# Kernel optimization log

Measured on AMD Instinct MI355X. Metric: run time of the kernel, lower is better.

## Reference

```python
import jax, jax.numpy as jnp
import numpy as np

QMAX = 127.0  # 8-bit symmetric: levels in [-128, 127]


def _ste_round(v):
    # round with straight-through estimator (matches torch fake-quant training)
    return v + jax.lax.stop_gradient(jnp.round(v) - v)


def _act_fake_quant(x, clip_factor):
    # per-tensor symmetric fake quant with learnable clip (lac):
    # clip range = sigmoid(clip_factor) * max|x|
    scale = jax.nn.sigmoid(clip_factor) * jnp.max(jnp.abs(x)) / QMAX
    return jnp.clip(_ste_round(x / scale), -QMAX - 1.0, QMAX) * scale


def _weight_fake_quant(w):
    # per-output-channel symmetric fake quant; w: [out, in]
    scale = jnp.max(jnp.abs(w), axis=1, keepdims=True) / QMAX
    return jnp.clip(_ste_round(w / scale), -QMAX - 1.0, QMAX) * scale


def setup_inputs() -> dict:
    key = jax.random.key(0)
    k1, k2, k3, k4 = jax.random.split(key, 4)
    B, S, H, I = 8, 8192, 1024, 2816
    return {
        "x": jax.random.normal(k1, (B, S, H), dtype=jnp.float32),
        "clip_x": jnp.full((1,), 4.0, dtype=jnp.float32),     # sigmoid(4) ~ 0.982
        "clip_down": jnp.full((1,), 4.0, dtype=jnp.float32),
        "w_gate": jax.random.normal(k2, (I, H), dtype=jnp.float32) * 0.02,
        "w_up": jax.random.normal(k3, (I, H), dtype=jnp.float32) * 0.02,
        "w_down": jax.random.normal(k4, (H, I), dtype=jnp.float32) * 0.02,
    }


def reference(x, clip_x, clip_down, w_gate, w_up, w_down):
    # _trans_forward: quantize act -> gate/up quant-matmul -> SwiGLU -> quantize -> down quant-matmul
    xq = _act_fake_quant(x, clip_x[0])                       # [B,S,H]
    gate = jnp.einsum("bsh,ih->bsi", xq, _weight_fake_quant(w_gate))
    up = jnp.einsum("bsh,ih->bsi", xq, _weight_fake_quant(w_up))
    h = _act_fake_quant(jax.nn.silu(gate) * up, clip_down[0])  # [B,S,I]
    return jnp.einsum("bsi,hi->bsh", h, _weight_fake_quant(w_down))
```

## Files before the change

kernel.cpp:

```cpp
#include <hip/hip_runtime.h>
#include <stdint.h>

typedef __attribute__((ext_vector_type(4))) int i32x4;

typedef const __attribute__((address_space(1))) void gvoid_t;
typedef __attribute__((address_space(3))) void lvoid_t;

#define GLD16(g, l) __builtin_amdgcn_global_load_lds((gvoid_t*)(g), (lvoid_t*)(l), 16, 0, 0)
#define FENCE() asm volatile("" ::: "memory")
#define BARRIER() do { FENCE(); __builtin_amdgcn_s_barrier(); FENCE(); } while (0)
#define SCHEDB() __builtin_amdgcn_sched_barrier(0)
#define GATE(n) asm volatile("s_waitcnt vmcnt(" #n ")\n\ts_barrier" ::: "memory")

__device__ inline int q1mul(float x, float r) {
    return (int)fminf(fmaxf(rintf(x * r), -128.f), 127.f);
}
__device__ inline int q1div(float x, float s) {
    return (int)fminf(fmaxf(rintf(x / s), -128.f), 127.f);
}
__device__ inline int pack4(float4 v, float r) {
    return (q1mul(v.x, r) & 255) | ((q1mul(v.y, r) & 255) << 8) |
           ((q1mul(v.z, r) & 255) << 16) | ((q1mul(v.w, r) & 255) << 24);
}

__global__ void k_absmax(const float* __restrict__ x, size_t n4, unsigned int* __restrict__ out) {
    size_t S = (size_t)gridDim.x * blockDim.x;
    size_t i = (size_t)blockIdx.x * blockDim.x + threadIdx.x;
    const float4* x4 = (const float4*)x;
    float m0 = 0.f, m1 = 0.f, m2 = 0.f, m3 = 0.f;
    for (; i + 3 * S < n4; i += 4 * S) {
        float4 v0 = x4[i], v1 = x4[i + S], v2 = x4[i + 2 * S], v3 = x4[i + 3 * S];
        m0 = fmaxf(m0, fmaxf(fmaxf(fabsf(v0.x), fabsf(v0.y)), fmaxf(fabsf(v0.z), fabsf(v0.w))));
        m1 = fmaxf(m1, fmaxf(fmaxf(fabsf(v1.x), fabsf(v1.y)), fmaxf(fabsf(v1.z), fabsf(v1.w))));
        m2 = fmaxf(m2, fmaxf(fmaxf(fabsf(v2.x), fabsf(v2.y)), fmaxf(fabsf(v2.z), fabsf(v2.w))));
        m3 = fmaxf(m3, fmaxf(fmaxf(fabsf(v3.x), fabsf(v3.y)), fmaxf(fabsf(v3.z), fabsf(v3.w))));
    }
    for (; i < n4; i += S) {
        float4 v = x4[i];
        m0 = fmaxf(m0, fmaxf(fmaxf(fabsf(v.x), fabsf(v.y)), fmaxf(fabsf(v.z), fabsf(v.w))));
    }
    float m = fmaxf(fmaxf(m0, m1), fmaxf(m2, m3));
    #pragma unroll
    for (int off = 32; off > 0; off >>= 1) m = fmaxf(m, __shfl_xor(m, off, 64));
    if ((threadIdx.x & 63) == 0) atomicMax(out, __float_as_uint(m));
}

__global__ void k_scale(const float* __restrict__ clip, const unsigned int* __restrict__ maxbits,
                        float* __restrict__ s_out) {
    float m = __uint_as_float(*maxbits);
    float sig = 1.f / (1.f + expf(-clip[0]));
    float s = sig * m / 127.f;
    s_out[0] = s;
    s_out[1] = 1.f / s;
}

__global__ void k_quant_f32_i8(const float* __restrict__ in, int4* __restrict__ out,
                               const float* __restrict__ sptr, size_t n16) {
    float r = sptr[1];
    size_t S = (size_t)gridDim.x * blockDim.x;
    size_t i = (size_t)blockIdx.x * blockDim.x + threadIdx.x;
    const float4* in4 = (const float4*)in;
    for (; i < n16; i += S) {
        float4 v0 = in4[4 * i], v1 = in4[4 * i + 1], v2 = in4[4 * i + 2], v3 = in4[4 * i + 3];
        int4 o;
        o.x = pack4(v0, r); o.y = pack4(v1, r); o.z = pack4(v2, r); o.w = pack4(v3, r);
        out[i] = o;
    }
}

__global__ void k_quant_h16_i8(const short* __restrict__ h16, const float* __restrict__ sblk,
                               const float* __restrict__ sh, int4* __restrict__ qh, size_t nchunks) {
    const float rh = sh[1] * (1.f / 32766.f);
    size_t S = (size_t)gridDim.x * blockDim.x;
    size_t i = (size_t)blockIdx.x * blockDim.x + threadIdx.x;
    for (; i < nchunks; i += S) {
        int row = (int)(i / 176);
        int col = (int)(i - (size_t)row * 176) * 16;
        float f = sblk[(row >> 8) * 22 + (col >> 7)] * rh;
        const int4* p = (const int4*)(h16 + (size_t)row * 2816 + col);
        int4 lo = p[0], hi = p[1];
        int w[8] = {lo.x, lo.y, lo.z, lo.w, hi.x, hi.y, hi.z, hi.w};
        int ob[4];
        #pragma unroll
        for (int j = 0; j < 4; ++j) {
            int q0 = q1mul((float)(short)(w[2 * j] & 0xFFFF), f);
            int q1 = q1mul((float)(short)(w[2 * j] >> 16), f);
            int q2 = q1mul((float)(short)(w[2 * j + 1] & 0xFFFF), f);
            int q3 = q1mul((float)(short)(w[2 * j + 1] >> 16), f);
            ob[j] = (q0 & 255) | ((q1 & 255) << 8) | ((q2 & 255) << 16) | ((q3 & 255) << 24);
        }
        int4 o; o.x = ob[0]; o.y = ob[1]; o.z = ob[2]; o.w = ob[3];
        qh[i] = o;
    }
}

__global__ void k_quant_w_i8(const float* __restrict__ W, int8_t* __restrict__ Q,
                             float* __restrict__ srow, int cols) {
    int row = blockIdx.x;
    const float* w = W + (size_t)row * cols;
    float m = 0.f;
    for (int c = threadIdx.x; c < cols; c += 256) m = fmaxf(m, fabsf(w[c]));
    #pragma unroll
    for (int off = 32; off > 0; off >>= 1) m = fmaxf(m, __shfl_xor(m, off, 64));
    __shared__ float red[4];
    if ((threadIdx.x & 63) == 0) red[threadIdx.x >> 6] = m;
    __syncthreads();
    if (threadIdx.x == 0) {
        float mm = fmaxf(fmaxf(red[0], red[1]), fmaxf(red[2], red[3]));
        red[0] = mm / 127.f;
        srow[row] = mm / 127.f;
    }
    __syncthreads();
    float s = red[0];
    for (int c = threadIdx.x; c < cols; c += 256)
        Q[(size_t)row * cols + c] = (int8_t)q1div(w[c], s);
}

#define MFMA_G1(AF, BG, BU, OFF)                                                              \
    _Pragma("unroll")                                                                         \
    for (int mi = 0; mi < 4; ++mi) {                                                          \
        _Pragma("unroll")                                                                     \
        for (int ni = 0; ni < 2; ++ni) {                                                      \
            accg[(OFF) + mi][ni] = __builtin_amdgcn_mfma_i32_16x16x64_i8(AF[mi], BG[ni], accg[(OFF) + mi][ni], 0, 0, 0); \
            accu[(OFF) + mi][ni] = __builtin_amdgcn_mfma_i32_16x16x64_i8(AF[mi], BU[ni], accu[(OFF) + mi][ni], 0, 0, 0); \
        }                                                                                     \
    }

__global__ __launch_bounds__(512, 2) void k_gemm1_i8(
    const int8_t* __restrict__ Aq, const int8_t* __restrict__ Bg, const int8_t* __restrict__ Bu,
    const float* __restrict__ sg, const float* __restrict__ su, const float* __restrict__ sx,
    short* __restrict__ H16, float* __restrict__ sblk, unsigned int* __restrict__ maxh,
    int nt_base)
{
    constexpr int K = 1024, N = 2816, NT = K / 128, BUF = 65536;
    __shared__ int8_t lds[2 * BUF];

    const int wgl = (int)blockIdx.x >> 3;
    const int xcd = (int)blockIdx.x & 7;
    const int mtspan = (int)(gridDim.x >> 3) / 11;
    const int mt = xcd * mtspan + wgl / 11;
    const int nt = nt_base + wgl % 11;
    const int m0 = mt * 256, n0 = nt * 128;
    const int tid = threadIdx.x;
    const int wid = tid >> 6, lane = tid & 63;
    const int wm = wid >> 2, wn = wid & 3;
    const int lr = lane & 15, lk = lane >> 4;

    const int srow = tid >> 2;
    const int scol = ((tid & 3) ^ ((srow >> 1) & 3)) << 4;
    const int8_t* gA0 = Aq + (size_t)(m0 + srow) * K + scol;
    const int8_t* gA1 = gA0 + (size_t)128 * K;
    const int8_t* gG  = Bg + (size_t)(n0 + srow) * K + scol;
    const int8_t* gU  = Bu + (size_t)(n0 + srow) * K + scol;
    const int ldst = wid << 10;

    const int swz = (lk ^ ((lr >> 1) & 3)) << 4;
    const int aoff = (wm * 128 + lr) * 64 + swz;
    const int boffG = 32768 + (wn * 32 + lr) * 64 + swz;
    const int boffU = 40960 + (wn * 32 + lr) * 64 + swz;

    i32x4 accg[8][2] = {};
    i32x4 accu[8][2] = {};
    i32x4 aA[4], aB[4], bgA[2], buA[2], bgB[2], buB[2];

    {
        int8_t* Lw = &lds[0];
        GLD16(gA0,      Lw + ldst);         GLD16(gA1,      Lw + 8192  + ldst);
        GLD16(gG,       Lw + 32768 + ldst); GLD16(gU,       Lw + 40960 + ldst);
        GLD16(gA0 + 64, Lw + 16384 + ldst); GLD16(gA1 + 64, Lw + 24576 + ldst);
        GLD16(gG  + 64, Lw + 49152 + ldst); GLD16(gU  + 64, Lw + 57344 + ldst);
    }
    GATE(4);
    {
        const int8_t* Lr = &lds[0];
        #pragma unroll
        for (int mi = 0; mi < 4; ++mi) aA[mi] = *(const i32x4*)(Lr + aoff + mi * 1024);
        #pragma unroll
        for (int ni = 0; ni < 2; ++ni) {
            bgA[ni] = *(const i32x4*)(Lr + boffG + ni * 1024);
            buA[ni] = *(const i32x4*)(Lr + boffU + ni * 1024);
        }
    }

    for (int t = 0; t < NT; ++t) {
        const bool st = (t + 1 < NT);
        const int8_t* Lr = &lds[(t & 1) * BUF];
        int8_t* Lw = &lds[((t + 1) & 1) * BUF];
        const size_t kk = (size_t)(t + 1) * 128;

        #pragma unroll
        for (int mi = 0; mi < 4; ++mi) aB[mi] = *(const i32x4*)(Lr + aoff + 4096 + mi * 1024);
        if (st) { GLD16(gA0 + kk, Lw + ldst); GLD16(gA1 + kk, Lw + 8192 + ldst); }
        SCHEDB();
        __builtin_amdgcn_s_setprio(1);
        MFMA_G1(aA, bgA, buA, 0);
        __builtin_amdgcn_s_setprio(0);
        if (st) { GATE(2); } else { GATE(0); }

        #pragma unroll
        for (int mi = 0; mi < 4; ++mi) aA[mi] = *(const i32x4*)(Lr + 16384 + aoff + mi * 1024);
        #pragma unroll
        for (int ni = 0; ni < 2; ++ni) {
            bgB[ni] = *(const i32x4*)(Lr + 16384 + boffG + ni * 1024);
            buB[ni] = *(const i32x4*)(Lr + 16384 + boffU + ni * 1024);
        }
        if (st) { GLD16(gG + kk, Lw + 32768 + ldst); GLD16(gU + kk, Lw + 40960 + ldst); }
        SCHEDB();
        __builtin_amdgcn_s_setprio(1);
        MFMA_G1(aB, bgA, buA, 4);
        __builtin_amdgcn_s_setprio(0);

        #pragma unroll
        for (int mi = 0; mi < 4; ++mi) aB[mi] = *(const i32x4*)(Lr + 16384 + aoff + 4096 + mi * 1024);
        if (st) { GLD16(gA0 + kk + 64, Lw + 16384 + ldst); GLD16(gA1 + kk + 64, Lw + 24576 + ldst);
                  GLD16(gG + kk + 64, Lw + 49152 + ldst);  GLD16(gU + kk + 64, Lw + 57344 + ldst); }
        SCHEDB();
        __builtin_amdgcn_s_setprio(1);
        MFMA_G1(aA, bgB, buB, 0);
        __builtin_amdgcn_s_setprio(0);
        if (st) { GATE(4); } else { GATE(0); }

        if (st) {
            #pragma unroll
            for (int mi = 0; mi < 4; ++mi) aA[mi] = *(const i32x4*)(Lw + aoff + mi * 1024);
            #pragma unroll
            for (int ni = 0; ni < 2; ++ni) {
                bgA[ni] = *(const i32x4*)(Lw + boffG + ni * 1024);
                buA[ni] = *(const i32x4*)(Lw + boffU + ni * 1024);
            }
        }
        SCHEDB();
        __builtin_amdgcn_s_setprio(1);
        MFMA_G1(aB, bgB, buB, 4);
        __builtin_amdgcn_s_setprio(0);
    }
    BARRIER();

    const float s_x = sx[0];
    float lmax = 0.f;
    #pragma unroll
    for (int ni = 0; ni < 2; ++ni) {
        const int nl = wn * 32 + ni * 16 + lr;
        const float fg = s_x * sg[n0 + nl];
        const float fu = s_x * su[n0 + nl];
        #pragma unroll
        for (int mi = 0; mi < 8; ++mi) {
            const int rowb = wm * 128 + mi * 16 + lk * 4;
            #pragma unroll
            for (int r = 0; r < 4; ++r) {
                float g = (float)accg[mi][ni][r] * fg;
                float u = (float)accu[mi][ni][r] * fu;
                float h = g * u / (1.f + expf(-g));
                *(float*)(lds + ((rowb + r) << 9) + (nl << 2)) = h;
                lmax = fmaxf(lmax, fabsf(h));
            }
        }
    }
    #pragma unroll
    for (int off = 32; off > 0; off >>= 1) lmax = fmaxf(lmax, __shfl_xor(lmax, off, 64));
    unsigned int* slot = (unsigned int*)&sblk[mt * 22 + nt];
    if (lane == 0) atomicMax(slot, __float_as_uint(lmax));
    BARRIER();
    const float bmax = __uint_as_float(*slot);
    if (tid == 0) atomicMax(maxh, __float_as_uint(bmax));
    const float qs = 32766.f / fmaxf(bmax, 1e-20f);
    uint* H16u = (uint*)H16;
    #pragma unroll
    for (int k = 0; k < 32; ++k) {
        const int fidx = 2 * (tid + k * 512);
        const int row = fidx >> 7, col = fidx & 127;
        const float2 hv = *(const float2*)(lds + (fidx << 2));
        const int s0 = (int)rintf(hv.x * qs), s1 = (int)rintf(hv.y * qs);
        H16u[((size_t)(m0 + row) * N + n0 + col) >> 1] = (s0 & 0xFFFF) | (s1 << 16);
    }
}

#define MFMA_G2(AF, BF, OFF)                                                                  \
    _Pragma("unroll")                                                                         \
    for (int mi = 0; mi < 4; ++mi) {                                                          \
        _Pragma("unroll")                                                                     \
        for (int ni = 0; ni < 4; ++ni)                                                        \
            acc[(OFF) + mi][ni] = __builtin_amdgcn_mfma_i32_16x16x64_i8(AF[mi], BF[ni], acc[(OFF) + mi][ni], 0, 0, 0); \
    }

__global__ __launch_bounds__(512, 2) void k_gemm2_i8(
    const int8_t* __restrict__ Aq, const int8_t* __restrict__ Bw,
    const float* __restrict__ sw, const float* __restrict__ sh,
    float* __restrict__ Out)
{
    constexpr int K = 2816, N = 1024, NT = K / 128, BUF = 65536;
    __shared__ int8_t lds[2 * BUF];

    const int chunk = gridDim.x >> 3;
    const int wg = ((int)blockIdx.x & 7) * chunk + ((int)blockIdx.x >> 3);
    const int mt = wg >> 2, nt = wg & 3;
    const int m0 = mt * 256, n0 = nt * 256;
    const int tid = threadIdx.x;
    const int wid = tid >> 6, lane = tid & 63;
    const int wm = wid >> 2, wn = wid & 3;
    const int lr = lane & 15, lk = lane >> 4;

    const int srow = tid >> 2;
    const int scol = ((tid & 3) ^ ((srow >> 1) & 3)) << 4;
    const int8_t* gA0 = Aq + (size_t)(m0 + srow) * K + scol;
    const int8_t* gA1 = gA0 + (size_t)128 * K;
    const int8_t* gB0 = Bw + (size_t)(n0 + srow) * K + scol;
    const int8_t* gB1 = gB0 + (size_t)128 * K;
    const int ldst = wid << 10;

    const int swz = (lk ^ ((lr >> 1) & 3)) << 4;
    const int aoff = (wm * 128 + lr) * 64 + swz;
    const int boff = 32768 + (wn * 64 + lr) * 64 + swz;

    i32x4 acc[8][4] = {};
    i32x4 aA[4], aB[4], bA[4], bB[4];

    {
        int8_t* Lw = &lds[0];
        GLD16(gA0,      Lw + ldst);         GLD16(gA1,      Lw + 8192  + ldst);
        GLD16(gB0,      Lw + 32768 + ldst); GLD16(gB1,      Lw + 40960 + ldst);
        GLD16(gA0 + 64, Lw + 16384 + ldst); GLD16(gA1 + 64, Lw + 24576 + ldst);
        GLD16(gB0 + 64, Lw + 49152 + ldst); GLD16(gB1 + 64, Lw + 57344 + ldst);
    }
    GATE(4);
    {
        const int8_t* Lr = &lds[0];
        #pragma unroll
        for (int mi = 0; mi < 4; ++mi) aA[mi] = *(const i32x4*)(Lr + aoff + mi * 1024);
        #pragma unroll
        for (int ni = 0; ni < 4; ++ni) bA[ni] = *(const i32x4*)(Lr + boff + ni * 1024);
    }

    for (int t = 0; t < NT; ++t) {
        const bool st = (t + 1 < NT);
        const int8_t* Lr = &lds[(t & 1) * BUF];
        int8_t* Lw = &lds[((t + 1) & 1) * BUF];
        const size_t kk = (size_t)(t + 1) * 128;

        #pragma unroll
        for (int mi = 0; mi < 4; ++mi) aB[mi] = *(const i32x4*)(Lr + aoff + 4096 + mi * 1024);
        if (st) { GLD16(gA0 + kk, Lw + ldst); GLD16(gA1 + kk, Lw + 8192 + ldst); }
        SCHEDB();
        __builtin_amdgcn_s_setprio(1);
        MFMA_G2(aA, bA, 0);
        __builtin_amdgcn_s_setprio(0);
        if (st) { GATE(2); } else { GATE(0); }

        #pragma unroll
        for (int mi = 0; mi < 4; ++mi) aA[mi] = *(const i32x4*)(Lr + 16384 + aoff + mi * 1024);
        #pragma unroll
        for (int ni = 0; ni < 4; ++ni) bB[ni] = *(const i32x4*)(Lr + 16384 + boff + ni * 1024);
        if (st) { GLD16(gB0 + kk, Lw + 32768 + ldst); GLD16(gB1 + kk, Lw + 40960 + ldst); }
        SCHEDB();
        __builtin_amdgcn_s_setprio(1);
        MFMA_G2(aB, bA, 4);
        __builtin_amdgcn_s_setprio(0);

        #pragma unroll
        for (int mi = 0; mi < 4; ++mi) aB[mi] = *(const i32x4*)(Lr + 16384 + aoff + 4096 + mi * 1024);
        if (st) { GLD16(gA0 + kk + 64, Lw + 16384 + ldst); GLD16(gA1 + kk + 64, Lw + 24576 + ldst);
                  GLD16(gB0 + kk + 64, Lw + 49152 + ldst); GLD16(gB1 + kk + 64, Lw + 57344 + ldst); }
        SCHEDB();
        __builtin_amdgcn_s_setprio(1);
        MFMA_G2(aA, bB, 0);
        __builtin_amdgcn_s_setprio(0);
        if (st) { GATE(4); } else { GATE(0); }

        if (st) {
            #pragma unroll
            for (int mi = 0; mi < 4; ++mi) aA[mi] = *(const i32x4*)(Lw + aoff + mi * 1024);
            #pragma unroll
            for (int ni = 0; ni < 4; ++ni) bA[ni] = *(const i32x4*)(Lw + boff + ni * 1024);
        }
        SCHEDB();
        __builtin_amdgcn_s_setprio(1);
        MFMA_G2(aB, bB, 4);
        __builtin_amdgcn_s_setprio(0);
    }

    const float s_h = sh[0];
    #pragma unroll
    for (int ni = 0; ni < 4; ++ni) {
        const int n = n0 + wn * 64 + ni * 16 + lr;
        const float f = s_h * sw[n];
        #pragma unroll
        for (int mi = 0; mi < 8; ++mi) {
            const int mb = m0 + wm * 128 + mi * 16 + lk * 4;
            #pragma unroll
            for (int r = 0; r < 4; ++r)
                Out[(size_t)(mb + r) * N + n] = (float)acc[mi][ni][r] * f;
        }
    }
}

extern "C" void kernel_launch(void* const* d_in, const int* in_sizes, int n_in,
                              void* d_out, int out_size, void* d_ws, size_t ws_size,
                              hipStream_t stream) {
    const float* x       = (const float*)d_in[0];
    const float* clip_x  = (const float*)d_in[1];
    const float* clip_dn = (const float*)d_in[2];
    const float* w_gate  = (const float*)d_in[3];
    const float* w_up    = (const float*)d_in[4];
    const float* w_down  = (const float*)d_in[5];
    float* out = (float*)d_out;

    const int Hd = 1024, Id = 2816;
    const int M = in_sizes[0] / Hd;
    const size_t nx = (size_t)M * Hd;
    const size_t nh = (size_t)M * Id;

    char* ws = (char*)d_ws;
    size_t off = 0;
    auto alloc = [&](size_t bytes) -> char* {
        char* p = ws + off;
        off = (off + bytes + 255) & ~(size_t)255;
        return p;
    };
    unsigned int* max_slots = (unsigned int*)alloc(8);
    float* sxp = (float*)alloc(8);
    float* shp = (float*)alloc(8);
    int8_t* qx  = (int8_t*)alloc(nx);
    int8_t* qwg = (int8_t*)alloc((size_t)Id * Hd);
    int8_t* qwu = (int8_t*)alloc((size_t)Id * Hd);
    int8_t* qwd = (int8_t*)alloc((size_t)Hd * Id);
    float* swg = (float*)alloc((size_t)Id * 4);
    float* swu = (float*)alloc((size_t)Id * 4);
    float* swd = (float*)alloc((size_t)Hd * 4);
    int8_t* qh = (int8_t*)alloc(nh);
    short* h16 = (short*)alloc(nh * 2);
    const size_t sblk_bytes = (size_t)(M / 256) * 22 * 4;
    float* sblk = (float*)alloc(sblk_bytes);

    hipMemsetAsync(max_slots, 0, 8, stream);
    hipMemsetAsync(sblk, 0, sblk_bytes, stream);

    k_absmax<<<4096, 256, 0, stream>>>(x, nx / 4, &max_slots[0]);
    k_scale<<<1, 1, 0, stream>>>(clip_x, &max_slots[0], sxp);
    k_quant_f32_i8<<<2048, 256, 0, stream>>>(x, (int4*)qx, sxp, nx / 16);
    k_quant_w_i8<<<Id, 256, 0, stream>>>(w_gate, qwg, swg, Hd);
    k_quant_w_i8<<<Id, 256, 0, stream>>>(w_up, qwu, swu, Hd);
    k_quant_w_i8<<<Hd, 256, 0, stream>>>(w_down, qwd, swd, Id);

    const int g1grid = (M / 256) * 11;
    k_gemm1_i8<<<g1grid, 512, 0, stream>>>(qx, qwg, qwu, swg, swu, sxp, h16, sblk, &max_slots[1], 0);
    k_gemm1_i8<<<g1grid, 512, 0, stream>>>(qx, qwg, qwu, swg, swu, sxp, h16, sblk, &max_slots[1], 11);
    k_scale<<<1, 1, 0, stream>>>(clip_dn, &max_slots[1], shp);
    k_quant_h16_i8<<<4096, 256, 0, stream>>>(h16, sblk, shp, (int4*)qh, nh / 16);

    k_gemm2_i8<<<(M / 256) * (Hd / 256), 512, 0, stream>>>(qh, qwd, swd, shp, out);
}
```

Before: 1.137 ms.

## Switch int8 GEMMs from 16x16x64 to 32x32x32 MFMA tiles

Both int8 GEMM kernels now use the 32x32x32 i8 MFMA instruction instead of 16x16x64. The LDS fragment addressing, the per-wave register tiling and the epilogue row/column mapping are rewritten to match the 32x32 output layout. Each operand fragment feeds more output per instruction, which is meant to cut the LDS reads and instruction count per FLOP. In exchange the epilogue store pattern changes and the new LDS read swizzle may bring bank conflicts.

```diff
diff --git a/kernel.cpp b/kernel.cpp
--- a/kernel.cpp
+++ b/kernel.cpp
@@ -2,6 +2,7 @@
 #include <stdint.h>
 
 typedef __attribute__((ext_vector_type(4))) int i32x4;
+typedef __attribute__((ext_vector_type(16))) int i32x16;
 
 typedef const __attribute__((address_space(1))) void gvoid_t;
 typedef __attribute__((address_space(3))) void lvoid_t;
@@ -116,14 +117,11 @@
         Q[(size_t)row * cols + c] = (int8_t)q1div(w[c], s);
 }
 
-#define MFMA_G1(AF, BG, BU, OFF)                                                              \
+#define MFMA8_G1(AF, BG, BU)                                                                  \
     _Pragma("unroll")                                                                         \
-    for (int mi = 0; mi < 4; ++mi) {                                                          \
-        _Pragma("unroll")                                                                     \
-        for (int ni = 0; ni < 2; ++ni) {                                                      \
-            accg[(OFF) + mi][ni] = __builtin_amdgcn_mfma_i32_16x16x64_i8(AF[mi], BG[ni], accg[(OFF) + mi][ni], 0, 0, 0); \
-            accu[(OFF) + mi][ni] = __builtin_amdgcn_mfma_i32_16x16x64_i8(AF[mi], BU[ni], accu[(OFF) + mi][ni], 0, 0, 0); \
-        }                                                                                     \
+    for (int m = 0; m < 4; ++m) {                                                             \
+        accg[m] = __builtin_amdgcn_mfma_i32_32x32x32_i8(AF[m], BG, accg[m], 0, 0, 0);         \
+        accu[m] = __builtin_amdgcn_mfma_i32_32x32x32_i8(AF[m], BU, accu[m], 0, 0, 0);         \
     }
 
 __global__ __launch_bounds__(512, 2) void k_gemm1_i8(
@@ -144,7 +142,8 @@
     const int tid = threadIdx.x;
     const int wid = tid >> 6, lane = tid & 63;
     const int wm = wid >> 2, wn = wid & 3;
-    const int lr = lane & 15, lk = lane >> 4;
+    const int l31 = lane & 31, l5 = lane >> 5;
+    const int lp = (l31 >> 1) & 3;
 
     const int srow = tid >> 2;
     const int scol = ((tid & 3) ^ ((srow >> 1) & 3)) << 4;
@@ -154,14 +153,18 @@
     const int8_t* gU  = Bu + (size_t)(n0 + srow) * K + scol;
     const int ldst = wid << 10;
 
-    const int swz = (lk ^ ((lr >> 1) & 3)) << 4;
-    const int aoff = (wm * 128 + lr) * 64 + swz;
-    const int boffG = 32768 + (wn * 32 + lr) * 64 + swz;
-    const int boffU = 40960 + (wn * 32 + lr) * 64 + swz;
-
-    i32x4 accg[8][2] = {};
-    i32x4 accu[8][2] = {};
-    i32x4 aA[4], aB[4], bgA[2], buA[2], bgB[2], buB[2];
+    const int F0 = ((l5 ^ lp) << 4);
+    const int F1 = (((2 + l5) ^ lp) << 4);
+    const int F2 = 16384 + F0, F3 = 16384 + F1;
+    int aR[4];
+    #pragma unroll
+    for (int m = 0; m < 4; ++m) aR[m] = (wm * 128 + m * 32 + l31) * 64;
+    const int bRg = 32768 + (wn * 32 + l31) * 64;
+    const int bRu = bRg + 8192;
+
+    i32x16 accg[4] = {};
+    i32x16 accu[4] = {};
+    i32x4 aA[4], aB[4], bgA, buA, bgB, buB;
 
     {
         int8_t* Lw = &lds[0];
@@ -174,12 +177,9 @@
     {
         const int8_t* Lr = &lds[0];
         #pragma unroll
-        for (int mi = 0; mi < 4; ++mi) aA[mi] = *(const i32x4*)(Lr + aoff + mi * 1024);
-        #pragma unroll
-        for (int ni = 0; ni < 2; ++ni) {
-            bgA[ni] = *(const i32x4*)(Lr + boffG + ni * 1024);
-            buA[ni] = *(const i32x4*)(Lr + boffU + ni * 1024);
-        }
+        for (int m = 0; m < 4; ++m) aA[m] = *(const i32x4*)(Lr + aR[m] + F0);
+        bgA = *(const i32x4*)(Lr + bRg + F0);
+        buA = *(const i32x4*)(Lr + bRu + F0);
     }
 
     for (int t = 0; t < NT; ++t) {
@@ -189,71 +189,66 @@
         const size_t kk = (size_t)(t + 1) * 128;
 
         #pragma unroll
-        for (int mi = 0; mi < 4; ++mi) aB[mi] = *(const i32x4*)(Lr + aoff + 4096 + mi * 1024);
+        for (int m = 0; m < 4; ++m) aB[m] = *(const i32x4*)(Lr + aR[m] + F1);
+        bgB = *(const i32x4*)(Lr + bRg + F1);
+        buB = *(const i32x4*)(Lr + bRu + F1);
         if (st) { GLD16(gA0 + kk, Lw + ldst); GLD16(gA1 + kk, Lw + 8192 + ldst); }
         SCHEDB();
         __builtin_amdgcn_s_setprio(1);
-        MFMA_G1(aA, bgA, buA, 0);
+        MFMA8_G1(aA, bgA, buA);
         __builtin_amdgcn_s_setprio(0);
         if (st) { GATE(2); } else { GATE(0); }
 
         #pragma unroll
-        for (int mi = 0; mi < 4; ++mi) aA[mi] = *(const i32x4*)(Lr + 16384 + aoff + mi * 1024);
-        #pragma unroll
-        for (int ni = 0; ni < 2; ++ni) {
-            bgB[ni] = *(const i32x4*)(Lr + 16384 + boffG + ni * 1024);
-            buB[ni] = *(const i32x4*)(Lr + 16384 + boffU + ni * 1024);
-        }
+        for (int m = 0; m < 4; ++m) aA[m] = *(const i32x4*)(Lr + aR[m] + F2);
+        bgA = *(const i32x4*)(Lr + bRg + F2);
+        buA = *(const i32x4*)(Lr + bRu + F2);
         if (st) { GLD16(gG + kk, Lw + 32768 + ldst); GLD16(gU + kk, Lw + 40960 + ldst); }
         SCHEDB();
         __builtin_amdgcn_s_setprio(1);
-        MFMA_G1(aB, bgA, buA, 4);
-        __builtin_amdgcn_s_setprio(0);
-
-        #pragma unroll
-        for (int mi = 0; mi < 4; ++mi) aB[mi] = *(const i32x4*)(Lr + 16384 + aoff + 4096 + mi * 1024);
+        MFMA8_G1(aB, bgB, buB);
+        __builtin_amdgcn_s_setprio(0);
+
+        #pragma unroll
+        for (int m = 0; m < 4; ++m) aB[m] = *(const i32x4*)(Lr + aR[m] + F3);
+        bgB = *(const i32x4*)(Lr + bRg + F3);
+        buB = *(const i32x4*)(Lr + bRu + F3);
         if (st) { GLD16(gA0 + kk + 64, Lw + 16384 + ldst); GLD16(gA1 + kk + 64, Lw + 24576 + ldst);
                   GLD16(gG + kk + 64, Lw + 49152 + ldst);  GLD16(gU + kk + 64, Lw + 57344 + ldst); }
         SCHEDB();
         __builtin_amdgcn_s_setprio(1);
-        MFMA_G1(aA, bgB, buB, 0);
+        MFMA8_G1(aA, bgA, buA);
         __builtin_amdgcn_s_setprio(0);
         if (st) { GATE(4); } else { GATE(0); }
 
         if (st) {
             #pragma unroll
-            for (int mi = 0; mi < 4; ++mi) aA[mi] = *(const i32x4*)(Lw + aoff + mi * 1024);
-            #pragma unroll
-            for (int ni = 0; ni < 2; ++ni) {
-                bgA[ni] = *(const i32x4*)(Lw + boffG + ni * 1024);
-                buA[ni] = *(const i32x4*)(Lw + boffU + ni * 1024);
-            }
+            for (int m = 0; m < 4; ++m) aA[m] = *(const i32x4*)(Lw + aR[m] + F0);
+            bgA = *(const i32x4*)(Lw + bRg + F0);
+            buA = *(const i32x4*)(Lw + bRu + F0);
         }
         SCHEDB();
         __builtin_amdgcn_s_setprio(1);
-        MFMA_G1(aB, bgB, buB, 4);
+        MFMA8_G1(aB, bgB, buB);
         __builtin_amdgcn_s_setprio(0);
     }
     BARRIER();
 
     const float s_x = sx[0];
+    const int col = wn * 32 + l31;
+    const float fg = s_x * sg[n0 + col];
+    const float fu = s_x * su[n0 + col];
     float lmax = 0.f;
     #pragma unroll
-    for (int ni = 0; ni < 2; ++ni) {
-        const int nl = wn * 32 + ni * 16 + lr;
-        const float fg = s_x * sg[n0 + nl];
-        const float fu = s_x * su[n0 + nl];
-        #pragma unroll
-        for (int mi = 0; mi < 8; ++mi) {
-            const int rowb = wm * 128 + mi * 16 + lk * 4;
-            #pragma unroll
-            for (int r = 0; r < 4; ++r) {
-                float g = (float)accg[mi][ni][r] * fg;
-                float u = (float)accu[mi][ni][r] * fu;
-                float h = g * u / (1.f + expf(-g));
-                *(float*)(lds + ((rowb + r) << 9) + (nl << 2)) = h;
-                lmax = fmaxf(lmax, fabsf(h));
-            }
+    for (int m = 0; m < 4; ++m) {
+        #pragma unroll
+        for (int r = 0; r < 16; ++r) {
+            const int row = wm * 128 + m * 32 + (r & 3) + 8 * (r >> 2) + 4 * l5;
+            float g = (float)accg[m][r] * fg;
+            float u = (float)accu[m][r] * fu;
+            float h = g * u / (1.f + expf(-g));
+            *(float*)(lds + (row << 9) + (col << 2)) = h;
+            lmax = fmaxf(lmax, fabsf(h));
         }
     }
     #pragma unroll
@@ -268,19 +263,18 @@
     #pragma unroll
     for (int k = 0; k < 32; ++k) {
         const int fidx = 2 * (tid + k * 512);
-        const int row = fidx >> 7, col = fidx & 127;
+        const int row = fidx >> 7, c2 = fidx & 127;
         const float2 hv = *(const float2*)(lds + (fidx << 2));
         const int s0 = (int)rintf(hv.x * qs), s1 = (int)rintf(hv.y * qs);
-        H16u[((size_t)(m0 + row) * N + n0 + col) >> 1] = (s0 & 0xFFFF) | (s1 << 16);
-    }
-}
-
-#define MFMA_G2(AF, BF, OFF)                                                                  \
+        H16u[((size_t)(m0 + row) * N + n0 + c2) >> 1] = (s0 & 0xFFFF) | (s1 << 16);
+    }
+}
+
+#define MFMA8_G2(AF, BF0, BF1)                                                                \
     _Pragma("unroll")                                                                         \
-    for (int mi = 0; mi < 4; ++mi) {                                                          \
-        _Pragma("unroll")                                                                     \
-        for (int ni = 0; ni < 4; ++ni)                                                        \
-            acc[(OFF) + mi][ni] = __builtin_amdgcn_mfma_i32_16x16x64_i8(AF[mi], BF[ni], acc[(OFF) + mi][ni], 0, 0, 0); \
+    for (int m = 0; m < 4; ++m) {                                                             \
+        acc0[m] = __builtin_amdgcn_mfma_i32_32x32x32_i8(AF[m], BF0, acc0[m], 0, 0, 0);        \
+        acc1[m] = __builtin_amdgcn_mfma_i32_32x32x32_i8(AF[m], BF1, acc1[m], 0, 0, 0);        \
     }
 
 __global__ __launch_bounds__(512, 2) void k_gemm2_i8(
@@ -298,7 +292,8 @@
     const int tid = threadIdx.x;
     const int wid = tid >> 6, lane = tid & 63;
     const int wm = wid >> 2, wn = wid & 3;
-    const int lr = lane & 15, lk = lane >> 4;
+    const int l31 = lane & 31, l5 = lane >> 5;
+    const int lp = (l31 >> 1) & 3;
 
     const int srow = tid >> 2;
     const int scol = ((tid & 3) ^ ((srow >> 1) & 3)) << 4;
@@ -308,12 +303,18 @@
     const int8_t* gB1 = gB0 + (size_t)128 * K;
     const int ldst = wid << 10;
 
-    const int swz = (lk ^ ((lr >> 1) & 3)) << 4;
-    const int aoff = (wm * 128 + lr) * 64 + swz;
-    const int boff = 32768 + (wn * 64 + lr) * 64 + swz;
-
-    i32x4 acc[8][4] = {};
-    i32x4 aA[4], aB[4], bA[4], bB[4];
+    const int F0 = ((l5 ^ lp) << 4);
+    const int F1 = (((2 + l5) ^ lp) << 4);
+    const int F2 = 16384 + F0, F3 = 16384 + F1;
+    int aR[4];
+    #pragma unroll
+    for (int m = 0; m < 4; ++m) aR[m] = (wm * 128 + m * 32 + l31) * 64;
+    const int bR0 = 32768 + (wn * 64 + l31) * 64;
+    const int bR1 = bR0 + 2048;
+
+    i32x16 acc0[4] = {};
+    i32x16 acc1[4] = {};
+    i32x4 aA[4], aB[4], b0A, b1A, b0B, b1B;
 
     {
         int8_t* Lw = &lds[0];
@@ -326,9 +327,9 @@
     {
         const int8_t* Lr = &lds[0];
         #pragma unroll
-        for (int mi = 0; mi < 4; ++mi) aA[mi] = *(const i32x4*)(Lr + aoff + mi * 1024);
-        #pragma unroll
-        for (int ni = 0; ni < 4; ++ni) bA[ni] = *(const i32x4*)(Lr + boff + ni * 1024);
+        for (int m = 0; m < 4; ++m) aA[m] = *(const i32x4*)(Lr + aR[m] + F0);
+        b0A = *(const i32x4*)(Lr + bR0 + F0);
+        b1A = *(const i32x4*)(Lr + bR1 + F0);
     }
 
     for (int t = 0; t < NT; ++t) {
@@ -338,57 +339,63 @@
         const size_t kk = (size_t)(t + 1) * 128;
 
         #pragma unroll
-        for (int mi = 0; mi < 4; ++mi) aB[mi] = *(const i32x4*)(Lr + aoff + 4096 + mi * 1024);
+        for (int m = 0; m < 4; ++m) aB[m] = *(const i32x4*)(Lr + aR[m] + F1);
+        b0B = *(const i32x4*)(Lr + bR0 + F1);
+        b1B = *(const i32x4*)(Lr + bR1 + F1);
         if (st) { GLD16(gA0 + kk, Lw + ldst); GLD16(gA1 + kk, Lw + 8192 + ldst); }
         SCHEDB();
         __builtin_amdgcn_s_setprio(1);
-        MFMA_G2(aA, bA, 0);
+        MFMA8_G2(aA, b0A, b1A);
         __builtin_amdgcn_s_setprio(0);
         if (st) { GATE(2); } else { GATE(0); }
 
         #pragma unroll
-        for (int mi = 0; mi < 4; ++mi) aA[mi] = *(const i32x4*)(Lr + 16384 + aoff + mi * 1024);
-        #pragma unroll
-        for (int ni = 0; ni < 4; ++ni) bB[ni] = *(const i32x4*)(Lr + 16384 + boff + ni * 1024);
+        for (int m = 0; m < 4; ++m) aA[m] = *(const i32x4*)(Lr + aR[m] + F2);
+        b0A = *(const i32x4*)(Lr + bR0 + F2);
+        b1A = *(const i32x4*)(Lr + bR1 + F2);
         if (st) { GLD16(gB0 + kk, Lw + 32768 + ldst); GLD16(gB1 + kk, Lw + 40960 + ldst); }
         SCHEDB();
         __builtin_amdgcn_s_setprio(1);
-        MFMA_G2(aB, bA, 4);
-        __builtin_amdgcn_s_setprio(0);
-
-        #pragma unroll
-        for (int mi = 0; mi < 4; ++mi) aB[mi] = *(const i32x4*)(Lr + 16384 + aoff + 4096 + mi * 1024);
+        MFMA8_G2(aB, b0B, b1B);
+        __builtin_amdgcn_s_setprio(0);
+
+        #pragma unroll
+        for (int m = 0; m < 4; ++m) aB[m] = *(const i32x4*)(Lr + aR[m] + F3);
+        b0B = *(const i32x4*)(Lr + bR0 + F3);
+        b1B = *(const i32x4*)(Lr + bR1 + F3);
         if (st) { GLD16(gA0 + kk + 64, Lw + 16384 + ldst); GLD16(gA1 + kk + 64, Lw + 24576 + ldst);
                   GLD16(gB0 + kk + 64, Lw + 49152 + ldst); GLD16(gB1 + kk + 64, Lw + 57344 + ldst); }
         SCHEDB();
         __builtin_amdgcn_s_setprio(1);
-        MFMA_G2(aA, bB, 0);
+        MFMA8_G2(aA, b0A, b1A);
         __builtin_amdgcn_s_setprio(0);
         if (st) { GATE(4); } else { GATE(0); }
 
         if (st) {
             #pragma unroll
-            for (int mi = 0; mi < 4; ++mi) aA[mi] = *(const i32x4*)(Lw + aoff + mi * 1024);
+            for (int m = 0; m < 4; ++m) aA[m] = *(const i32x4*)(Lw + aR[m] + F0);
+            b0A = *(const i32x4*)(Lw + bR0 + F0);
+            b1A = *(const i32x4*)(Lw + bR1 + F0);
+        }
+        SCHEDB();
+        __builtin_amdgcn_s_setprio(1);
+        MFMA8_G2(aB, b0B, b1B);
+        __builtin_amdgcn_s_setprio(0);
+    }
+
+    const float s_h = sh[0];
+    #pragma unroll
+    for (int nb = 0; nb < 2; ++nb) {
+        const int n = n0 + wn * 64 + nb * 32 + l31;
+        const float f = s_h * sw[n];
+        #pragma unroll
+        for (int m = 0; m < 4; ++m) {
             #pragma unroll
-            for (int ni = 0; ni < 4; ++ni) bA[ni] = *(const i32x4*)(Lw + boff + ni * 1024);
-        }
-        SCHEDB();
-        __builtin_amdgcn_s_setprio(1);
-        MFMA_G2(aB, bB, 4);
-        __builtin_amdgcn_s_setprio(0);
-    }
-
-    const float s_h = sh[0];
-    #pragma unroll
-    for (int ni = 0; ni < 4; ++ni) {
-        const int n = n0 + wn * 64 + ni * 16 + lr;
-        const float f = s_h * sw[n];
-        #pragma unroll
-        for (int mi = 0; mi < 8; ++mi) {
-            const int mb = m0 + wm * 128 + mi * 16 + lk * 4;
-            #pragma unroll
-            for (int r = 0; r < 4; ++r)
-                Out[(size_t)(mb + r) * N + n] = (float)acc[mi][ni][r] * f;
+            for (int r = 0; r < 16; ++r) {
+                const int row = m0 + wm * 128 + m * 32 + (r & 3) + 8 * (r >> 2) + 4 * l5;
+                const int v = nb ? acc1[m][r] : acc0[m][r];
+                Out[(size_t)row * N + n] = (float)v * f;
+            }
         }
     }
 }
```

Measured after the change: 1.168 ms. +2.8%, slower.
